# Optimization experiments

Measured on AMD Instinct MI355X. Metric: run time of the kernel, lower is better.

## Reference

```python
import jax, jax.numpy as jnp
import numpy as np

N, E, D = 20000, 320000, 128


def _glorot(key, shape):
    fan_in, fan_out = shape[0], shape[-1]
    lim = jnp.sqrt(6.0 / (fan_in + fan_out)).astype(jnp.float32)
    return jax.random.uniform(key, shape, jnp.float32, -lim, lim)


def setup_inputs() -> dict:
    key = jax.random.key(0)
    ks = jax.random.split(key, 16)
    h = jax.random.normal(ks[0], (N, 1, D), jnp.float32)
    x = jax.random.normal(ks[1], (N, 3), jnp.float32)
    edge_index = jax.random.randint(ks[2], (2, E), 0, N, jnp.int64)
    # edge_mlp: SPDMLP(2D -> D -> D), 2 linear layers with ReLU between
    W1e = _glorot(ks[3], (2 * D, D)); b1e = jnp.zeros((D,), jnp.float32)
    W2e = _glorot(ks[4], (D, D));     b2e = jnp.zeros((D,), jnp.float32)
    # edge_inf: Linear(D, 1) + Sigmoid
    Wg = _glorot(ks[5], (D, 1));      bg = jnp.zeros((1,), jnp.float32)
    # node_mlp: SPDMLP(2D -> D -> D)
    W1n = _glorot(ks[6], (2 * D, D)); b1n = jnp.zeros((D,), jnp.float32)
    W2n = _glorot(ks[7], (D, D));     b2n = jnp.zeros((D,), jnp.float32)
    return {"h": h, "x": x, "edge_index": edge_index,
            "W1e": W1e, "b1e": b1e, "W2e": W2e, "b2e": b2e,
            "Wg": Wg, "bg": bg,
            "W1n": W1n, "b1n": b1n, "W2n": W2n, "b2n": b2n}


def _feature_joint(a, b):
    # a: [B, Na, Da], b: [B, Nb, Db] -> [B, Na+Nb, Da+Db] block-diagonal concat
    Da, Db = a.shape[2], b.shape[2]
    a_exp = jnp.concatenate([a, jnp.zeros(a.shape[:2] + (Db,), a.dtype)], axis=2)
    b_exp = jnp.concatenate([jnp.zeros(b.shape[:2] + (Da,), b.dtype), b], axis=2)
    return jnp.concatenate([a_exp, b_exp], axis=1)


def _mlp2(y, W1, b1, W2, b2):
    return jax.nn.relu(y @ W1 + b1) @ W2 + b2


def reference(h, x, edge_index, W1e, b1e, W2e, b2e, Wg, bg, W1n, b1n, W2n, b2n):
    src, dst = edge_index[0], edge_index[1]
    hi, hj = h[dst], h[src]                              # [E, 1, D] each
    mij = _mlp2(_feature_joint(hi, hj), W1e, b1e, W2e, b2e)  # [E, 2, D]
    eij = jax.nn.sigmoid(mij @ Wg + bg)                  # [E, 2, 1]
    mi = jax.ops.segment_sum(mij * eij, dst, num_segments=h.shape[0])  # [N, 2, D]
    h_new = h + _mlp2(_feature_joint(mi, h), W1n, b1n, W2n, b2n)       # [N, 3, D]
    return (h_new, x)
```

## Files before the change

### kernel.cpp

```cpp
#include <hip/hip_runtime.h>

#define D    128
#define SP   136
#define FS   132
#define NC   2
#define CAP  64

typedef __attribute__((ext_vector_type(8))) short bf16x8;
typedef __attribute__((ext_vector_type(4))) float f32x4;
typedef unsigned short u16;

__device__ __forceinline__ float sigmoidf(float v) { return 1.0f / (1.0f + __expf(-v)); }

__device__ __forceinline__ u16 f2bf(float x) {
    union { float f; unsigned u; } c; c.f = x;
    return (u16)((c.u + 0x7fffu + ((c.u >> 16) & 1u)) >> 16);
}
__device__ __forceinline__ float bflo(unsigned u) {
    union { unsigned v; float f; } c; c.v = u << 16; return c.f;
}
__device__ __forceinline__ float bfhi(unsigned u) {
    union { unsigned v; float f; } c; c.v = u & 0xffff0000u; return c.f;
}
__device__ __forceinline__ void acc8(float* a, uint4 q) {
    a[0] += bflo(q.x); a[1] += bfhi(q.x);
    a[2] += bflo(q.y); a[3] += bfhi(q.y);
    a[4] += bflo(q.z); a[5] += bfhi(q.z);
    a[6] += bflo(q.w); a[7] += bfhi(q.w);
}

__device__ __forceinline__ void layer32(
    const u16* __restrict__ plane, const short* __restrict__ WbM,
    int lane, int ctbase, f32x4 acc[NC][2])
{
    #pragma unroll
    for (int ks = 0; ks < 4; ++ks) {
        bf16x8 a[2];
        #pragma unroll
        for (int rt = 0; rt < 2; ++rt)
            a[rt] = *reinterpret_cast<const bf16x8*>(
                plane + (rt * 16 + (lane & 15)) * SP + ks * 32 + (lane >> 4) * 8);
        #pragma unroll
        for (int c = 0; c < NC; ++c) {
            const bf16x8 b = *reinterpret_cast<const bf16x8*>(
                WbM + ((ctbase + c) * 4 + ks) * 512 + lane * 8);
            #pragma unroll
            for (int rt = 0; rt < 2; ++rt)
                acc[c][rt] = __builtin_amdgcn_mfma_f32_16x16x32_bf16(a[rt], b, acc[c][rt], 0, 0, 0);
        }
    }
}

__device__ __forceinline__ void store_t32(
    const f32x4 acc[NC][2], const float b1v[NC],
    u16* __restrict__ dst, int lane, int ctbase)
{
    #pragma unroll
    for (int c = 0; c < NC; ++c)
        #pragma unroll
        for (int rt = 0; rt < 2; ++rt)
            #pragma unroll
            for (int rr = 0; rr < 4; ++rr)
                dst[(rt * 16 + (lane >> 4) * 4 + rr) * SP + (ctbase + c) * 16 + (lane & 15)] =
                    f2bf(fmaxf(acc[c][rt][rr] + b1v[c], 0.f));
}

__device__ __forceinline__ void stage32(
    const float* __restrict__ src, int base, int N, int tid, u16* __restrict__ plane)
{
    #pragma unroll
    for (int it = 0; it < 4; ++it) {
        const int idx = it * 256 + tid;
        const int row = idx >> 5, c4 = (idx & 31) << 2;
        int node = base + row; if (node >= N) node = N - 1;
        const float4 v = *reinterpret_cast<const float4*>(&src[(size_t)node * D + c4]);
        ushort4 s;
        s.x = f2bf(v.x); s.y = f2bf(v.y); s.z = f2bf(v.z); s.w = f2bf(v.w);
        *reinterpret_cast<ushort4*>(&plane[row * SP + c4]) = s;
    }
}

__device__ __forceinline__ void mlp_tail(
    const short* __restrict__ Wb, int mA,
    const float* __restrict__ b1n, const float* __restrict__ b2n,
    const float* __restrict__ h, float* __restrict__ out_h,
    int r, int base, int N,
    u16* __restrict__ P1, u16* __restrict__ P2, u16* __restrict__ smem)
{
    const int tid = threadIdx.x, lane = tid & 63, w = tid >> 6;
    const int ctbase = w * NC;

    float b1v[NC], b2v[NC];
    #pragma unroll
    for (int c = 0; c < NC; ++c) {
        const int j = (ctbase + c) * 16 + (lane & 15);
        b1v[c] = b1n[j]; b2v[c] = b2n[j];
    }

    f32x4 acc[NC][2];
    #pragma unroll
    for (int c = 0; c < NC; ++c)
        #pragma unroll
        for (int rt = 0; rt < 2; ++rt) acc[c][rt] = (f32x4){0.f, 0.f, 0.f, 0.f};
    layer32(P1, Wb + (size_t)mA * 16384, lane, ctbase, acc);
    store_t32(acc, b1v, P2, lane, ctbase);
    __syncthreads();

    f32x4 o[NC][2];
    #pragma unroll
    for (int c = 0; c < NC; ++c)
        #pragma unroll
        for (int rt = 0; rt < 2; ++rt) o[c][rt] = (f32x4){0.f, 0.f, 0.f, 0.f};
    layer32(P2, Wb + (size_t)5 * 16384, lane, ctbase, o);
    __syncthreads();

    float* fs = reinterpret_cast<float*>(smem);
    #pragma unroll
    for (int c = 0; c < NC; ++c)
        #pragma unroll
        for (int rt = 0; rt < 2; ++rt)
            #pragma unroll
            for (int rr = 0; rr < 4; ++rr)
                fs[(rt * 16 + (lane >> 4) * 4 + rr) * FS + (ctbase + c) * 16 + (lane & 15)] =
                    o[c][rt][rr] + b2v[c];
    __syncthreads();

    const int nl = tid >> 3, cg = tid & 7;
    const int node = base + nl;
    if (node < N) {
        #pragma unroll
        for (int k = 0; k < 4; ++k) {
            float4 ov = *reinterpret_cast<const float4*>(&fs[nl * FS + cg * 16 + k * 4]);
            const float4 hv = *reinterpret_cast<const float4*>(&h[(size_t)node * D + cg * 16 + k * 4]);
            ov.x += hv.x; ov.y += hv.y; ov.z += hv.z; ov.w += hv.w;
            *reinterpret_cast<float4*>(&out_h[((size_t)node * 3 + r) * D + cg * 16 + k * 4]) = ov;
        }
    }
}

__global__ __launch_bounds__(256) void zero_repack_kernel(
    int* __restrict__ cnt, int N, int ZB,
    const float* __restrict__ W1e, const float* __restrict__ W2e,
    const float* __restrict__ W1n, const float* __restrict__ W2n,
    short* __restrict__ Wb)
{
    if (blockIdx.x < (unsigned)ZB) {
        const int i = blockIdx.x * 256 + threadIdx.x;
        if (i < N) cnt[i] = 0;
        return;
    }
    const int gid = (blockIdx.x - ZB) * 256 + threadIdx.x;
    if (gid >= 6 * 8 * 4 * 64) return;
    const int lane = gid & 63;
    int t = gid >> 6;
    const int ks = t & 3; t >>= 2;
    const int ct = t & 7;
    const int m  = t >> 3;
    const float* src;
    switch (m) {
        case 0: src = W1e;             break;
        case 1: src = W1e + 128 * 128; break;
        case 2: src = W2e;             break;
        case 3: src = W1n;             break;
        case 4: src = W1n + 128 * 128; break;
        default: src = W2n;            break;
    }
    const int j  = ct * 16 + (lane & 15);
    const int k0 = ks * 32 + (lane >> 4) * 8;
    bf16x8 hi;
    #pragma unroll
    for (int e = 0; e < 8; ++e) hi[e] = (short)f2bf(src[(size_t)(k0 + e) * 128 + j]);
    *reinterpret_cast<bf16x8*>(Wb + (size_t)m * 16384 + (ct * 4 + ks) * 512 + lane * 8) = hi;
}

__global__ __launch_bounds__(256, 4) void k2_pre_scatter(
    const float* __restrict__ h, const short* __restrict__ Wb,
    const float* __restrict__ b1e, const float* __restrict__ b2e,
    const float* __restrict__ Wg,  const float* __restrict__ bg,
    u16* __restrict__ Q1b,
    int N, int QB,
    const int* __restrict__ ei, int E, int* __restrict__ cnt, int* __restrict__ bucket)
{
    __shared__ __align__(16) u16 smem[2 * 32 * SP];
    __shared__ float red_s[4][32];
    u16* P1 = smem;
    u16* P2 = smem + 32 * SP;

    const unsigned bid = blockIdx.x;
    const int tid = threadIdx.x, lane = tid & 63, w = tid >> 6;

    if (bid >= (unsigned)QB) {
        const int e0 = (bid - QB) * 1024 + tid;
        #pragma unroll
        for (int k = 0; k < 4; ++k) {
            const int e = e0 + k * 256;
            if (e < E) {
                const int s = ei[e];
                const int d = ei[E + e];
                const int slot = atomicAdd(&cnt[d], 1);
                if (slot < CAP) bucket[(size_t)d * CAP + slot] = s;
            }
        }
        return;
    }

    const int base = bid * 32;
    const int ctbase = w * NC;
    stage32(h, base, N, tid, P1);
    __syncthreads();

    float b1v[NC], b2v[NC], wgv[NC];
    #pragma unroll
    for (int c = 0; c < NC; ++c) {
        const int j = (ctbase + c) * 16 + (lane & 15);
        b1v[c] = b1e[j]; b2v[c] = b2e[j]; wgv[c] = Wg[j];
    }
    const float bgv = bg[0];

    f32x4 acc[NC][2];
    #pragma unroll
    for (int c = 0; c < NC; ++c)
        #pragma unroll
        for (int rt = 0; rt < 2; ++rt) acc[c][rt] = (f32x4){0.f, 0.f, 0.f, 0.f};
    layer32(P1, Wb + (size_t)1 * 16384, lane, ctbase, acc);
    store_t32(acc, b1v, P2, lane, ctbase);
    __syncthreads();

    f32x4 p[NC][2];
    #pragma unroll
    for (int c = 0; c < NC; ++c)
        #pragma unroll
        for (int rt = 0; rt < 2; ++rt) p[c][rt] = (f32x4){0.f, 0.f, 0.f, 0.f};
    layer32(P2, Wb + (size_t)2 * 16384, lane, ctbase, p);

    #pragma unroll
    for (int rt = 0; rt < 2; ++rt)
        #pragma unroll
        for (int rr = 0; rr < 4; ++rr) {
            float part = 0.f;
            #pragma unroll
            for (int c = 0; c < NC; ++c) part += (p[c][rt][rr] + b2v[c]) * wgv[c];
            #pragma unroll
            for (int m = 1; m <= 8; m <<= 1) part += __shfl_xor(part, m, 64);
            if ((lane & 15) == 0)
                red_s[w][rt * 16 + (lane >> 4) * 4 + rr] = part;
        }
    __syncthreads();

    #pragma unroll
    for (int rt = 0; rt < 2; ++rt)
        #pragma unroll
        for (int rr = 0; rr < 4; ++rr) {
            const int row = rt * 16 + (lane >> 4) * 4 + rr;
            const float g = sigmoidf(red_s[0][row] + red_s[1][row] +
                                     red_s[2][row] + red_s[3][row] + bgv);
            #pragma unroll
            for (int c = 0; c < NC; ++c)
                P1[row * SP + (ctbase + c) * 16 + (lane & 15)] =
                    f2bf((p[c][rt][rr] + b2v[c]) * g);
        }
    __syncthreads();

    const int nl = tid >> 3, cg = tid & 7;
    const int node = base + nl;
    if (node < N) {
        const uint4 v0 = *reinterpret_cast<const uint4*>(&P1[nl * SP + cg * 16]);
        const uint4 v1 = *reinterpret_cast<const uint4*>(&P1[nl * SP + cg * 16 + 8]);
        *reinterpret_cast<uint4*>(&Q1b[(size_t)node * D + cg * 16])     = v0;
        *reinterpret_cast<uint4*>(&Q1b[(size_t)node * D + cg * 16 + 8]) = v1;
    }
}

__global__ __launch_bounds__(256, 4) void k3_r1_r0_r2(
    const float* __restrict__ h,  const u16* __restrict__ Q1b,
    const short* __restrict__ Wb,
    const float* __restrict__ b1e, const float* __restrict__ b2e,
    const float* __restrict__ Wg,  const float* __restrict__ bg,
    const float* __restrict__ b1n, const float* __restrict__ b2n,
    const int* __restrict__ cnt,  const int* __restrict__ bucket,
    const float* __restrict__ x,  float* __restrict__ out_x,
    float* __restrict__ out_h, int N, int RT)
{
    __shared__ __align__(16) u16 smem[2 * 32 * SP];
    __shared__ float red_s[4][32];
    u16* P1 = smem;
    u16* P2 = smem + 32 * SP;

    const int tid = threadIdx.x, lane = tid & 63, w = tid >> 6;
    const int ctbase = w * NC;

    if (blockIdx.x < (unsigned)RT) {
        const int base = blockIdx.x * 32;
        const int nl = tid >> 3, cg = tid & 7;
        int node = base + nl; if (node >= N) node = N - 1;
        int deg = cnt[node]; if (deg > CAP) deg = CAP;
        const int* __restrict__ bk = bucket + (size_t)node * CAP;
        const u16* __restrict__ Qc = Q1b + cg * 16;
        float a[16] = {0.f,0.f,0.f,0.f,0.f,0.f,0.f,0.f,0.f,0.f,0.f,0.f,0.f,0.f,0.f,0.f};
        int i = 0;
        for (; i + 1 < deg; i += 2) {
            const int s0 = bk[i], s1 = bk[i + 1];
            const uint4 qa0 = *reinterpret_cast<const uint4*>(Qc + (size_t)s0 * D);
            const uint4 qb0 = *reinterpret_cast<const uint4*>(Qc + (size_t)s0 * D + 8);
            const uint4 qa1 = *reinterpret_cast<const uint4*>(Qc + (size_t)s1 * D);
            const uint4 qb1 = *reinterpret_cast<const uint4*>(Qc + (size_t)s1 * D + 8);
            acc8(a, qa0); acc8(a + 8, qb0);
            acc8(a, qa1); acc8(a + 8, qb1);
        }
        if (i < deg) {
            const int s = bk[i];
            const uint4 qa = *reinterpret_cast<const uint4*>(Qc + (size_t)s * D);
            const uint4 qb = *reinterpret_cast<const uint4*>(Qc + (size_t)s * D + 8);
            acc8(a, qa); acc8(a + 8, qb);
        }
        #pragma unroll
        for (int k4 = 0; k4 < 4; ++k4) {
            ushort4 s4;
            s4.x = f2bf(a[k4 * 4 + 0]); s4.y = f2bf(a[k4 * 4 + 1]);
            s4.z = f2bf(a[k4 * 4 + 2]); s4.w = f2bf(a[k4 * 4 + 3]);
            *reinterpret_cast<ushort4*>(&P1[nl * SP + cg * 16 + k4 * 4]) = s4;
        }
        __syncthreads();
        mlp_tail(Wb, 3, b1n, b2n, h, out_h, 1, base, N, P1, P2, smem);
        return;
    }

    if (blockIdx.x >= (unsigned)(2 * RT)) {
        const int tile = blockIdx.x - 2 * RT;
        const int base = tile * 32;
        {
            const int xi = tile * 96 + tid;
            if (tid < 96 && xi < N * 3) out_x[xi] = x[xi];
        }
        stage32(h, base, N, tid, P1);
        __syncthreads();
        mlp_tail(Wb, 4, b1n, b2n, h, out_h, 2, base, N, P1, P2, smem);
        return;
    }

    const int base = (blockIdx.x - RT) * 32;
    stage32(h, base, N, tid, P1);
    __syncthreads();

    float b1v[NC], b2v[NC], wgv[NC];
    #pragma unroll
    for (int c = 0; c < NC; ++c) {
        const int j = (ctbase + c) * 16 + (lane & 15);
        b1v[c] = b1e[j]; b2v[c] = b2e[j]; wgv[c] = Wg[j];
    }
    const float bgv = bg[0];

    f32x4 acc[NC][2];
    #pragma unroll
    for (int c = 0; c < NC; ++c)
        #pragma unroll
        for (int rt = 0; rt < 2; ++rt) acc[c][rt] = (f32x4){0.f, 0.f, 0.f, 0.f};
    layer32(P1, Wb, lane, ctbase, acc);
    store_t32(acc, b1v, P2, lane, ctbase);
    __syncthreads();

    f32x4 p[NC][2];
    #pragma unroll
    for (int c = 0; c < NC; ++c)
        #pragma unroll
        for (int rt = 0; rt < 2; ++rt) p[c][rt] = (f32x4){0.f, 0.f, 0.f, 0.f};
    layer32(P2, Wb + (size_t)2 * 16384, lane, ctbase, p);

    #pragma unroll
    for (int rt = 0; rt < 2; ++rt)
        #pragma unroll
        for (int rr = 0; rr < 4; ++rr) {
            float part = 0.f;
            #pragma unroll
            for (int c = 0; c < NC; ++c) part += (p[c][rt][rr] + b2v[c]) * wgv[c];
            #pragma unroll
            for (int m = 1; m <= 8; m <<= 1) part += __shfl_xor(part, m, 64);
            if ((lane & 15) == 0)
                red_s[w][rt * 16 + (lane >> 4) * 4 + rr] = part;
        }
    __syncthreads();

    #pragma unroll
    for (int rt = 0; rt < 2; ++rt)
        #pragma unroll
        for (int rr = 0; rr < 4; ++rr) {
            const int row = rt * 16 + (lane >> 4) * 4 + rr;
            const float g = sigmoidf(red_s[0][row] + red_s[1][row] +
                                     red_s[2][row] + red_s[3][row] + bgv);
            int node2 = base + row; if (node2 >= N) node2 = N - 1;
            const float cv = (float)cnt[node2];
            #pragma unroll
            for (int c = 0; c < NC; ++c)
                P1[row * SP + (ctbase + c) * 16 + (lane & 15)] =
                    f2bf(cv * (p[c][rt][rr] + b2v[c]) * g);
        }
    __syncthreads();
    mlp_tail(Wb, 3, b1n, b2n, h, out_h, 0, base, N, P1, P2, smem);
}

extern "C" void kernel_launch(void* const* d_in, const int* in_sizes, int n_in,
                              void* d_out, int out_size, void* d_ws, size_t ws_size,
                              hipStream_t stream)
{
    const float* h   = (const float*)d_in[0];
    const float* x   = (const float*)d_in[1];
    const int*   ei  = (const int*)d_in[2];
    const float* W1e = (const float*)d_in[3];
    const float* b1e = (const float*)d_in[4];
    const float* W2e = (const float*)d_in[5];
    const float* b2e = (const float*)d_in[6];
    const float* Wg  = (const float*)d_in[7];
    const float* bg  = (const float*)d_in[8];
    const float* W1n = (const float*)d_in[9];
    const float* b1n = (const float*)d_in[10];
    const float* W2n = (const float*)d_in[11];
    const float* b2n = (const float*)d_in[12];

    const int N = in_sizes[0] / D;
    const int E = in_sizes[2] / 2;

    u16*   Q1b    = (u16*)d_ws;
    short* Wb     = (short*)(Q1b + (size_t)N * D);
    int*   cnt    = (int*)(Wb + 6 * 16384);
    int*   bucket = cnt + N;

    float* out_h = (float*)d_out;
    float* out_x = out_h + (size_t)N * 3 * D;

    const int nt = (N + 31) / 32;
    const int ZB = (N + 255) / 256;
    const int RB = 48;
    const int QB = nt;
    const int SB = (E + 1023) / 1024;

    zero_repack_kernel<<<ZB + RB, 256, 0, stream>>>(cnt, N, ZB, W1e, W2e, W1n, W2n, Wb);
    k2_pre_scatter<<<QB + SB, 256, 0, stream>>>(h, Wb, b1e, b2e, Wg, bg, Q1b,
                                                N, QB, ei, E, cnt, bucket);
    k3_r1_r0_r2<<<nt * 3, 256, 0, stream>>>(h, Q1b, Wb, b1e, b2e, Wg, bg,
                                            b1n, b2n, cnt, bucket, x, out_x,
                                            out_h, N, nt);
}
```

Baseline: 60.01 us.

## Move independent h-row node MLP into pre-scatter kernel and unroll gather by four

The node-MLP work for the h rows, which does not depend on the aggregated messages, now runs in the second kernel alongside the edge pre-MLP and the edge bucketing. This balances work across launches and shortens the dependent third kernel. The x copy moves along with it. Separately, the neighbor gather loop is unrolled from two to four edges per iteration to keep more loads in flight, at some cost in register pressure.

```diff
diff --git a/kernel.cpp b/kernel.cpp
--- a/kernel.cpp
+++ b/kernel.cpp
@@ -173,12 +173,14 @@
     *reinterpret_cast<bf16x8*>(Wb + (size_t)m * 16384 + (ct * 4 + ks) * 512 + lane * 8) = hi;
 }
 
-__global__ __launch_bounds__(256, 4) void k2_pre_scatter(
+__global__ __launch_bounds__(256, 4) void k2_pre_r2_scatter(
     const float* __restrict__ h, const short* __restrict__ Wb,
     const float* __restrict__ b1e, const float* __restrict__ b2e,
     const float* __restrict__ Wg,  const float* __restrict__ bg,
-    u16* __restrict__ Q1b,
-    int N, int QB,
+    const float* __restrict__ b1n, const float* __restrict__ b2n,
+    u16* __restrict__ Q1b, float* __restrict__ out_h,
+    const float* __restrict__ x,  float* __restrict__ out_x,
+    int N, int QB, int MB,
     const int* __restrict__ ei, int E, int* __restrict__ cnt, int* __restrict__ bucket)
 {
     __shared__ __align__(16) u16 smem[2 * 32 * SP];
@@ -189,8 +191,8 @@
     const unsigned bid = blockIdx.x;
     const int tid = threadIdx.x, lane = tid & 63, w = tid >> 6;
 
-    if (bid >= (unsigned)QB) {
-        const int e0 = (bid - QB) * 1024 + tid;
+    if (bid >= (unsigned)(QB + MB)) {
+        const int e0 = (bid - QB - MB) * 1024 + tid;
         #pragma unroll
         for (int k = 0; k < 4; ++k) {
             const int e = e0 + k * 256;
@@ -204,6 +206,19 @@
         return;
     }
 
+    if (bid >= (unsigned)QB) {
+        const int tile = bid - QB;
+        const int base = tile * 32;
+        {
+            const int xi = tile * 96 + tid;
+            if (tid < 96 && xi < N * 3) out_x[xi] = x[xi];
+        }
+        stage32(h, base, N, tid, P1);
+        __syncthreads();
+        mlp_tail(Wb, 4, b1n, b2n, h, out_h, 2, base, N, P1, P2, smem);
+        return;
+    }
+
     const int base = bid * 32;
     const int ctbase = w * NC;
     stage32(h, base, N, tid, P1);
@@ -271,14 +286,13 @@
     }
 }
 
-__global__ __launch_bounds__(256, 4) void k3_r1_r0_r2(
+__global__ __launch_bounds__(256, 4) void k3_r1_r0(
     const float* __restrict__ h,  const u16* __restrict__ Q1b,
     const short* __restrict__ Wb,
     const float* __restrict__ b1e, const float* __restrict__ b2e,
     const float* __restrict__ Wg,  const float* __restrict__ bg,
     const float* __restrict__ b1n, const float* __restrict__ b2n,
     const int* __restrict__ cnt,  const int* __restrict__ bucket,
-    const float* __restrict__ x,  float* __restrict__ out_x,
     float* __restrict__ out_h, int N, int RT)
 {
     __shared__ __align__(16) u16 smem[2 * 32 * SP];
@@ -298,16 +312,22 @@
         const u16* __restrict__ Qc = Q1b + cg * 16;
         float a[16] = {0.f,0.f,0.f,0.f,0.f,0.f,0.f,0.f,0.f,0.f,0.f,0.f,0.f,0.f,0.f,0.f};
         int i = 0;
-        for (; i + 1 < deg; i += 2) {
-            const int s0 = bk[i], s1 = bk[i + 1];
+        for (; i + 3 < deg; i += 4) {
+            const int s0 = bk[i], s1 = bk[i + 1], s2 = bk[i + 2], s3 = bk[i + 3];
             const uint4 qa0 = *reinterpret_cast<const uint4*>(Qc + (size_t)s0 * D);
             const uint4 qb0 = *reinterpret_cast<const uint4*>(Qc + (size_t)s0 * D + 8);
             const uint4 qa1 = *reinterpret_cast<const uint4*>(Qc + (size_t)s1 * D);
             const uint4 qb1 = *reinterpret_cast<const uint4*>(Qc + (size_t)s1 * D + 8);
+            const uint4 qa2 = *reinterpret_cast<const uint4*>(Qc + (size_t)s2 * D);
+            const uint4 qb2 = *reinterpret_cast<const uint4*>(Qc + (size_t)s2 * D + 8);
+            const uint4 qa3 = *reinterpret_cast<const uint4*>(Qc + (size_t)s3 * D);
+            const uint4 qb3 = *reinterpret_cast<const uint4*>(Qc + (size_t)s3 * D + 8);
             acc8(a, qa0); acc8(a + 8, qb0);
             acc8(a, qa1); acc8(a + 8, qb1);
-        }
-        if (i < deg) {
+            acc8(a, qa2); acc8(a + 8, qb2);
+            acc8(a, qa3); acc8(a + 8, qb3);
+        }
+        for (; i < deg; ++i) {
             const int s = bk[i];
             const uint4 qa = *reinterpret_cast<const uint4*>(Qc + (size_t)s * D);
             const uint4 qb = *reinterpret_cast<const uint4*>(Qc + (size_t)s * D + 8);
@@ -322,19 +342,6 @@
         }
         __syncthreads();
         mlp_tail(Wb, 3, b1n, b2n, h, out_h, 1, base, N, P1, P2, smem);
-        return;
-    }
-
-    if (blockIdx.x >= (unsigned)(2 * RT)) {
-        const int tile = blockIdx.x - 2 * RT;
-        const int base = tile * 32;
-        {
-            const int xi = tile * 96 + tid;
-            if (tid < 96 && xi < N * 3) out_x[xi] = x[xi];
-        }
-        stage32(h, base, N, tid, P1);
-        __syncthreads();
-        mlp_tail(Wb, 4, b1n, b2n, h, out_h, 2, base, N, P1, P2, smem);
         return;
     }
 
@@ -431,12 +438,13 @@
     const int ZB = (N + 255) / 256;
     const int RB = 48;
     const int QB = nt;
+    const int MB = nt;
     const int SB = (E + 1023) / 1024;
 
     zero_repack_kernel<<<ZB + RB, 256, 0, stream>>>(cnt, N, ZB, W1e, W2e, W1n, W2n, Wb);
-    k2_pre_scatter<<<QB + SB, 256, 0, stream>>>(h, Wb, b1e, b2e, Wg, bg, Q1b,
-                                                N, QB, ei, E, cnt, bucket);
-    k3_r1_r0_r2<<<nt * 3, 256, 0, stream>>>(h, Q1b, Wb, b1e, b2e, Wg, bg,
-                                            b1n, b2n, cnt, bucket, x, out_x,
-                                            out_h, N, nt);
-}
+    k2_pre_r2_scatter<<<QB + MB + SB, 256, 0, stream>>>(h, Wb, b1e, b2e, Wg, bg,
+                                                        b1n, b2n, Q1b, out_h, x, out_x,
+                                                        N, QB, MB, ei, E, cnt, bucket);
+    k3_r1_r0<<<nt * 2, 256, 0, stream>>>(h, Q1b, Wb, b1e, b2e, Wg, bg,
+                                         b1n, b2n, cnt, bucket, out_h, N, nt);
+}
```

Measured after the change: 58.32 us. 1.03x faster.
